# Performance work log

Hardware: AMD Instinct MI355X
Metric: run time of the kernel (lower is better)

## Reference

```python
import jax, jax.numpy as jnp
import numpy as np

N_NODES = 50000
N_EDGES = 800000
D_FEAT = 128


def setup_inputs() -> dict:
    key = jax.random.key(0)
    k1, k2, k3, k4 = jax.random.split(key, 4)
    edge_index = jax.random.randint(k1, (2, N_EDGES), 0, N_NODES, dtype=jnp.int64 if jax.config.jax_enable_x64 else jnp.int32)
    edge_vals = jax.random.uniform(k2, (N_EDGES,), dtype=jnp.float32)
    features = jax.random.normal(k3, (N_NODES, D_FEAT), dtype=jnp.float32)
    bias = jax.random.normal(k4, (D_FEAT,), dtype=jnp.float32)
    return {"edge_index": edge_index, "edge_vals": edge_vals, "features": features, "bias": bias}


def reference(edge_index, edge_vals, features, bias):
    # SpMM: out[dst] += A[dst, src] * X[src], i.e. sparse adjacency @ dense features
    src = edge_index[0]
    dst = edge_index[1]
    msg = features[src] * edge_vals[:, None]          # [E, D] gather + scale
    out = jax.ops.segment_sum(msg, dst, num_segments=features.shape[0])  # [N, D] scatter-add
    return out + bias                                  # fused bias add
```

## Files before the change

kernel.cpp:

```cpp
#include <hip/hip_runtime.h>
#include <hip/hip_bf16.h>

#define D_FEAT 128
#define D4 (D_FEAT / 4)
#define BKT_SHIFT 7
#define BKT_NODES 128
#define NCHUNK 256
#define MAXBKT 512
#define CAP 3072

__global__ __launch_bounds__(256) void k1_hist_cvt(
        const int* __restrict__ dst, int E, int chunk, int nbkt,
        int* __restrict__ M, int Mpad,
        const float4* __restrict__ fin, __hip_bfloat162* __restrict__ fout,
        int n4) {
    int c = blockIdx.x;
    int tid = threadIdx.x;
    if (c < NCHUNK) {
        __shared__ int hist[MAXBKT];
        for (int i = tid; i < nbkt; i += 256) hist[i] = 0;
        __syncthreads();
        int lo = c * chunk;
        int hi = min(lo + chunk, E);
        for (int i = lo + tid; i < hi; i += 256)
            atomicAdd(&hist[dst[i] >> BKT_SHIFT], 1);
        __syncthreads();
        for (int i = tid; i < nbkt; i += 256)
            M[i * NCHUNK + c] = hist[i];
        if (c == 0) {
            for (int i = nbkt * NCHUNK + tid; i < Mpad; i += 256) M[i] = 0;
        }
    } else {
        int nb = gridDim.x - NCHUNK;
        int idx = (c - NCHUNK) * 256 + tid;
        int stride = nb * 256;
        for (int i = idx; i < n4; i += stride) {
            float4 f = fin[i];
            fout[2 * i + 0] = __float22bfloat162_rn(make_float2(f.x, f.y));
            fout[2 * i + 1] = __float22bfloat162_rn(make_float2(f.z, f.w));
        }
    }
}

__global__ __launch_bounds__(1024) void k2a_scan(int* __restrict__ M,
                                                 int* __restrict__ bsum) {
    __shared__ int s[1024];
    int tid = threadIdx.x;
    int j = blockIdx.x * 1024 + tid;
    int v = M[j];
    s[tid] = v;
    __syncthreads();
    for (int off = 1; off < 1024; off <<= 1) {
        int t = (tid >= off) ? s[tid - off] : 0;
        __syncthreads();
        s[tid] += t;
        __syncthreads();
    }
    M[j] = s[tid] - v;
    if (tid == 1023) bsum[blockIdx.x] = s[1023];
}

__global__ void k2b_scan(int* __restrict__ bsum, int nb) {
    __shared__ int s[256];
    int tid = threadIdx.x;
    int v = (tid < nb) ? bsum[tid] : 0;
    s[tid] = v;
    __syncthreads();
    for (int off = 1; off < 256; off <<= 1) {
        int t = (tid >= off) ? s[tid - off] : 0;
        __syncthreads();
        s[tid] += t;
        __syncthreads();
    }
    if (tid < nb) bsum[tid] = s[tid] - v;
    if (tid == 255) bsum[nb] = s[255];
}

__global__ __launch_bounds__(512) void k3_partition(
        const int* __restrict__ src, const int* __restrict__ dst,
        const float* __restrict__ vals, int E, int chunk, int nbkt,
        const int* __restrict__ M, const int* __restrict__ bsum,
        int2* __restrict__ spackA) {
    __shared__ int lcur[MAXBKT];
    int c = blockIdx.x;
    int tid = threadIdx.x;
    for (int i = tid; i < nbkt; i += 512) {
        int j = i * NCHUNK + c;
        lcur[i] = M[j] + bsum[j >> 10];
    }
    __syncthreads();
    int lo = c * chunk;
    int hi = min(lo + chunk, E);
    for (int i = lo + tid; i < hi; i += 512) {
        int d = dst[i];
        int s = src[i];
        float v = vals[i];
        int pos = atomicAdd(&lcur[d >> BKT_SHIFT], 1);
        spackA[pos] = make_int2((s & 0xFFFF) | ((d & (BKT_NODES - 1)) << 16),
                                __float_as_int(v));
    }
}

__global__ __launch_bounds__(1024) void k45_sort_gather(
        const int* __restrict__ M, const int* __restrict__ bsum,
        const int2* __restrict__ spackA, int2* __restrict__ spackB,
        const __hip_bfloat162* __restrict__ feat,
        const float2* __restrict__ bias2, float2* __restrict__ out2,
        int N, int nbkt) {
    __shared__ int hist[BKT_NODES];
    __shared__ int sbuf[BKT_NODES];
    __shared__ int lcur[BKT_NODES];
    __shared__ int2 ls[CAP];
    int b = blockIdx.x;
    int tid = threadIdx.x;
    int j0 = b * NCHUNK;
    int j1 = (b + 1) * NCHUNK;
    int base = M[j0] + bsum[j0 >> 10];
    int end  = M[j1] + bsum[j1 >> 10];
    int cnt = end - base;
    bool inlds = (cnt <= CAP);

    if (tid < BKT_NODES) hist[tid] = 0;
    __syncthreads();
    for (int i = tid; i < cnt; i += 1024)
        atomicAdd(&hist[(spackA[base + i].x >> 16) & (BKT_NODES - 1)], 1);
    __syncthreads();
    if (tid < BKT_NODES) sbuf[tid] = hist[tid];
    __syncthreads();
    for (int off = 1; off < BKT_NODES; off <<= 1) {
        int t = (tid < BKT_NODES && tid >= off) ? sbuf[tid - off] : 0;
        __syncthreads();
        if (tid < BKT_NODES) sbuf[tid] += t;
        __syncthreads();
    }
    if (tid < BKT_NODES) lcur[tid] = sbuf[tid] - hist[tid];
    __syncthreads();
    for (int i = tid; i < cnt; i += 1024) {
        int2 r = spackA[base + i];
        int p = atomicAdd(&lcur[(r.x >> 16) & (BKT_NODES - 1)], 1);
        if (inlds) ls[p] = r;
        else       spackB[base + p] = r;
    }
    __syncthreads();

    int wave = tid >> 6, lane = tid & 63;
    float2 bv = bias2[lane];
    for (int n = wave; n < BKT_NODES; n += 16) {
        int node = (b << BKT_SHIFT) + n;
        if (node >= N) break;
        int lbeg = sbuf[n] - hist[n];
        int lend = sbuf[n];
        float2 acc0 = bv;
        float2 acc1 = make_float2(0.f, 0.f);
        int e = lbeg;
        if (inlds) {
            for (; e + 8 <= lend; e += 8) {
                int2 p[8];
                __hip_bfloat162 h[8];
#pragma unroll
                for (int j = 0; j < 8; j++) p[j] = ls[e + j];
#pragma unroll
                for (int j = 0; j < 8; j++)
                    h[j] = feat[(size_t)(p[j].x & 0xFFFF) * 64 + lane];
#pragma unroll
                for (int j = 0; j < 8; j++) {
                    float v = __int_as_float(p[j].y);
                    float2 f = __bfloat1622float2(h[j]);
                    if (j & 1) { acc1.x += v * f.x; acc1.y += v * f.y; }
                    else       { acc0.x += v * f.x; acc0.y += v * f.y; }
                }
            }
            for (; e < lend; e++) {
                int2 p = ls[e];
                float v = __int_as_float(p.y);
                float2 f = __bfloat1622float2(feat[(size_t)(p.x & 0xFFFF) * 64 + lane]);
                acc0.x += v * f.x; acc0.y += v * f.y;
            }
        } else {
            for (; e + 8 <= lend; e += 8) {
                int2 p[8];
                __hip_bfloat162 h[8];
#pragma unroll
                for (int j = 0; j < 8; j++) p[j] = spackB[base + e + j];
#pragma unroll
                for (int j = 0; j < 8; j++)
                    h[j] = feat[(size_t)(p[j].x & 0xFFFF) * 64 + lane];
#pragma unroll
                for (int j = 0; j < 8; j++) {
                    float v = __int_as_float(p[j].y);
                    float2 f = __bfloat1622float2(h[j]);
                    if (j & 1) { acc1.x += v * f.x; acc1.y += v * f.y; }
                    else       { acc0.x += v * f.x; acc0.y += v * f.y; }
                }
            }
            for (; e < lend; e++) {
                int2 p = spackB[base + e];
                float v = __int_as_float(p.y);
                float2 f = __bfloat1622float2(feat[(size_t)(p.x & 0xFFFF) * 64 + lane]);
                acc0.x += v * f.x; acc0.y += v * f.y;
            }
        }
        acc0.x += acc1.x; acc0.y += acc1.y;
        out2[(size_t)node * 64 + lane] = acc0;
    }
}


__global__ void init_bias_kernel(float4* __restrict__ out,
                                 const float4* __restrict__ bias, int n4) {
    int i = blockIdx.x * blockDim.x + threadIdx.x;
    if (i < n4) out[i] = bias[i & (D4 - 1)];
}

__global__ void spmm_edge_kernel(const int* __restrict__ src,
                                 const int* __restrict__ dst,
                                 const float* __restrict__ vals,
                                 const float4* __restrict__ feat,
                                 float* __restrict__ out, int n_edges) {
    int tid = blockIdx.x * blockDim.x + threadIdx.x;
    int e = tid >> 5;
    int lane = tid & 31;
    if (e >= n_edges) return;
    int s = src[e];
    int d = dst[e];
    float v = vals[e];
    float4 f = feat[(size_t)s * D4 + lane];
    float* o = out + (size_t)d * D_FEAT + lane * 4;
    atomicAdd(o + 0, v * f.x);
    atomicAdd(o + 1, v * f.y);
    atomicAdd(o + 2, v * f.z);
    atomicAdd(o + 3, v * f.w);
}

extern "C" void kernel_launch(void* const* d_in, const int* in_sizes, int n_in,
                              void* d_out, int out_size, void* d_ws, size_t ws_size,
                              hipStream_t stream) {
    const int* edge_index = (const int*)d_in[0];
    const float* edge_vals = (const float*)d_in[1];
    const float* features  = (const float*)d_in[2];
    const float* bias      = (const float*)d_in[3];

    int E = in_sizes[1];
    int N = in_sizes[2] / D_FEAT;
    const int* src = edge_index;
    const int* dst = edge_index + E;
    float* out = (float*)d_out;

    int nbkt = (N + BKT_NODES - 1) >> BKT_SHIFT;
    int n4 = N * D_FEAT / 4;
    int chunk = (E + NCHUNK - 1) / NCHUNK;
    int Mpad = ((nbkt * NCHUNK + 1 + 1023) / 1024) * 1024;
    int nblk2 = Mpad / 1024;

    size_t fb_bytes = (size_t)N * D_FEAT * 2;
    size_t sp_bytes = (size_t)E * 8;
    size_t needed = fb_bytes + 2 * sp_bytes +
                    ((size_t)Mpad + (nblk2 + 1)) * 4;

    bool ok = (ws_size >= needed) && (N >= 1) && (N <= 65536) && (E >= 1) &&
              (in_sizes[3] == D_FEAT) && (nbkt <= MAXBKT) && (nblk2 <= 256);

    if (ok) {
        char* wp = (char*)d_ws;
        __hip_bfloat162* fb16 = (__hip_bfloat162*)wp;  wp += fb_bytes;
        int2* spackA = (int2*)wp;                      wp += sp_bytes;
        int2* spackB = (int2*)wp;                      wp += sp_bytes;
        int* M       = (int*)wp;                       wp += (size_t)Mpad * 4;
        int* bsum    = (int*)wp;

        k1_hist_cvt<<<NCHUNK + 256, 256, 0, stream>>>(dst, E, chunk, nbkt,
                                                      M, Mpad,
                                                      (const float4*)features,
                                                      fb16, n4);
        k2a_scan<<<nblk2, 1024, 0, stream>>>(M, bsum);
        k2b_scan<<<1, 256, 0, stream>>>(bsum, nblk2);
        k3_partition<<<NCHUNK, 512, 0, stream>>>(src, dst, edge_vals, E, chunk,
                                                 nbkt, M, bsum, spackA);
        k45_sort_gather<<<nbkt, 1024, 0, stream>>>(M, bsum, spackA, spackB,
                                                   fb16, (const float2*)bias,
                                                   (float2*)out, N, nbkt);
    } else {
        int no4 = out_size / 4;
        {
            int block = 256, grid = (no4 + block - 1) / block;
            init_bias_kernel<<<grid, block, 0, stream>>>((float4*)out,
                                                         (const float4*)bias, no4);
        }
        {
            int block = 256;
            long long total = (long long)E * 32;
            int grid = (int)((total + block - 1) / block);
            spmm_edge_kernel<<<grid, block, 0, stream>>>(src, dst, edge_vals,
                                                         (const float4*)features,
                                                         out, E);
        }
    }
}
```

Baseline: 145.6 us.

## Fold bucket prefix scan into partition kernel, dropping two scan launches

Removes the two separate scan kernels. Each partition block now reads the full chunk-by-bucket histogram (stored chunk-major, MAXBKT wide), computes bucket totals and its own chunk prefix, and does a block-level scan to get bucket offsets. Block 0 publishes global bucket bases for the sort/gather kernel. This cuts two kernel launches and their serialization, in exchange for every partition block redundantly reading 256x512 histogram entries and scanning them.

```diff
diff --git a/kernel.cpp b/kernel.cpp
--- a/kernel.cpp
+++ b/kernel.cpp
@@ -10,26 +10,24 @@
 #define CAP 3072
 
 __global__ __launch_bounds__(256) void k1_hist_cvt(
-        const int* __restrict__ dst, int E, int chunk, int nbkt,
-        int* __restrict__ M, int Mpad,
+        const int* __restrict__ dst, int E, int nbkt,
+        int* __restrict__ M,
         const float4* __restrict__ fin, __hip_bfloat162* __restrict__ fout,
         int n4) {
     int c = blockIdx.x;
     int tid = threadIdx.x;
     if (c < NCHUNK) {
         __shared__ int hist[MAXBKT];
-        for (int i = tid; i < nbkt; i += 256) hist[i] = 0;
-        __syncthreads();
+        for (int i = tid; i < MAXBKT; i += 256) hist[i] = 0;
+        __syncthreads();
+        int chunk = (E + NCHUNK - 1) / NCHUNK;
         int lo = c * chunk;
         int hi = min(lo + chunk, E);
         for (int i = lo + tid; i < hi; i += 256)
             atomicAdd(&hist[dst[i] >> BKT_SHIFT], 1);
         __syncthreads();
-        for (int i = tid; i < nbkt; i += 256)
-            M[i * NCHUNK + c] = hist[i];
-        if (c == 0) {
-            for (int i = nbkt * NCHUNK + tid; i < Mpad; i += 256) M[i] = 0;
-        }
+        for (int i = tid; i < MAXBKT; i += 256)
+            M[c * MAXBKT + i] = hist[i];
     } else {
         int nb = gridDim.x - NCHUNK;
         int idx = (c - NCHUNK) * 256 + tid;
@@ -42,67 +40,50 @@
     }
 }
 
-__global__ __launch_bounds__(1024) void k2a_scan(int* __restrict__ M,
-                                                 int* __restrict__ bsum) {
-    __shared__ int s[1024];
-    int tid = threadIdx.x;
-    int j = blockIdx.x * 1024 + tid;
-    int v = M[j];
-    s[tid] = v;
-    __syncthreads();
-    for (int off = 1; off < 1024; off <<= 1) {
-        int t = (tid >= off) ? s[tid - off] : 0;
-        __syncthreads();
-        s[tid] += t;
-        __syncthreads();
-    }
-    M[j] = s[tid] - v;
-    if (tid == 1023) bsum[blockIdx.x] = s[1023];
-}
-
-__global__ void k2b_scan(int* __restrict__ bsum, int nb) {
-    __shared__ int s[256];
-    int tid = threadIdx.x;
-    int v = (tid < nb) ? bsum[tid] : 0;
-    s[tid] = v;
-    __syncthreads();
-    for (int off = 1; off < 256; off <<= 1) {
-        int t = (tid >= off) ? s[tid - off] : 0;
-        __syncthreads();
-        s[tid] += t;
-        __syncthreads();
-    }
-    if (tid < nb) bsum[tid] = s[tid] - v;
-    if (tid == 255) bsum[nb] = s[255];
-}
-
 __global__ __launch_bounds__(512) void k3_partition(
         const int* __restrict__ src, const int* __restrict__ dst,
-        const float* __restrict__ vals, int E, int chunk, int nbkt,
-        const int* __restrict__ M, const int* __restrict__ bsum,
+        const float* __restrict__ vals, int E, int nbkt,
+        const int* __restrict__ M, int* __restrict__ gbase,
         int2* __restrict__ spackA) {
+    __shared__ int s[MAXBKT];
     __shared__ int lcur[MAXBKT];
     int c = blockIdx.x;
     int tid = threadIdx.x;
-    for (int i = tid; i < nbkt; i += 512) {
-        int j = i * NCHUNK + c;
-        lcur[i] = M[j] + bsum[j >> 10];
-    }
-    __syncthreads();
+    int tot = 0, pre = 0;
+    for (int cc = 0; cc < NCHUNK; ++cc) {
+        int m = M[cc * MAXBKT + tid];
+        tot += m;
+        pre += (cc < c) ? m : 0;
+    }
+    s[tid] = tot;
+    __syncthreads();
+    for (int off = 1; off < MAXBKT; off <<= 1) {
+        int t = (tid >= off) ? s[tid - off] : 0;
+        __syncthreads();
+        s[tid] += t;
+        __syncthreads();
+    }
+    int incl = s[tid];
+    int base = incl - tot;
+    lcur[tid] = base + pre;
+    if (c == 0) {
+        if (tid < nbkt) gbase[tid] = base;
+        if (tid == MAXBKT - 1) gbase[nbkt] = incl;
+    }
+    __syncthreads();
+    int chunk = (E + NCHUNK - 1) / NCHUNK;
     int lo = c * chunk;
     int hi = min(lo + chunk, E);
     for (int i = lo + tid; i < hi; i += 512) {
         int d = dst[i];
-        int s = src[i];
-        float v = vals[i];
         int pos = atomicAdd(&lcur[d >> BKT_SHIFT], 1);
-        spackA[pos] = make_int2((s & 0xFFFF) | ((d & (BKT_NODES - 1)) << 16),
-                                __float_as_int(v));
+        spackA[pos] = make_int2((src[i] & 0xFFFF) | ((d & (BKT_NODES - 1)) << 16),
+                                __float_as_int(vals[i]));
     }
 }
 
 __global__ __launch_bounds__(1024) void k45_sort_gather(
-        const int* __restrict__ M, const int* __restrict__ bsum,
+        const int* __restrict__ gbase,
         const int2* __restrict__ spackA, int2* __restrict__ spackB,
         const __hip_bfloat162* __restrict__ feat,
         const float2* __restrict__ bias2, float2* __restrict__ out2,
@@ -113,10 +94,8 @@
     __shared__ int2 ls[CAP];
     int b = blockIdx.x;
     int tid = threadIdx.x;
-    int j0 = b * NCHUNK;
-    int j1 = (b + 1) * NCHUNK;
-    int base = M[j0] + bsum[j0 >> 10];
-    int end  = M[j1] + bsum[j1 >> 10];
+    int base = gbase[b];
+    int end  = gbase[b + 1];
     int cnt = end - base;
     bool inlds = (cnt <= CAP);
 
@@ -248,35 +227,29 @@
 
     int nbkt = (N + BKT_NODES - 1) >> BKT_SHIFT;
     int n4 = N * D_FEAT / 4;
-    int chunk = (E + NCHUNK - 1) / NCHUNK;
-    int Mpad = ((nbkt * NCHUNK + 1 + 1023) / 1024) * 1024;
-    int nblk2 = Mpad / 1024;
 
     size_t fb_bytes = (size_t)N * D_FEAT * 2;
     size_t sp_bytes = (size_t)E * 8;
-    size_t needed = fb_bytes + 2 * sp_bytes +
-                    ((size_t)Mpad + (nblk2 + 1)) * 4;
+    size_t m_bytes  = (size_t)NCHUNK * MAXBKT * 4;
+    size_t needed = fb_bytes + 2 * sp_bytes + m_bytes + (MAXBKT + 1) * 4;
 
     bool ok = (ws_size >= needed) && (N >= 1) && (N <= 65536) && (E >= 1) &&
-              (in_sizes[3] == D_FEAT) && (nbkt <= MAXBKT) && (nblk2 <= 256);
+              (in_sizes[3] == D_FEAT) && (nbkt <= MAXBKT);
 
     if (ok) {
         char* wp = (char*)d_ws;
         __hip_bfloat162* fb16 = (__hip_bfloat162*)wp;  wp += fb_bytes;
         int2* spackA = (int2*)wp;                      wp += sp_bytes;
         int2* spackB = (int2*)wp;                      wp += sp_bytes;
-        int* M       = (int*)wp;                       wp += (size_t)Mpad * 4;
-        int* bsum    = (int*)wp;
-
-        k1_hist_cvt<<<NCHUNK + 256, 256, 0, stream>>>(dst, E, chunk, nbkt,
-                                                      M, Mpad,
+        int* M       = (int*)wp;                       wp += m_bytes;
+        int* gbase   = (int*)wp;
+
+        k1_hist_cvt<<<NCHUNK + 256, 256, 0, stream>>>(dst, E, nbkt, M,
                                                       (const float4*)features,
                                                       fb16, n4);
-        k2a_scan<<<nblk2, 1024, 0, stream>>>(M, bsum);
-        k2b_scan<<<1, 256, 0, stream>>>(bsum, nblk2);
-        k3_partition<<<NCHUNK, 512, 0, stream>>>(src, dst, edge_vals, E, chunk,
-                                                 nbkt, M, bsum, spackA);
-        k45_sort_gather<<<nbkt, 1024, 0, stream>>>(M, bsum, spackA, spackB,
+        k3_partition<<<NCHUNK, 512, 0, stream>>>(src, dst, edge_vals, E,
+                                                 nbkt, M, gbase, spackA);
+        k45_sort_gather<<<nbkt, 1024, 0, stream>>>(gbase, spackA, spackB,
                                                    fb16, (const float2*)bias,
                                                    (float2*)out, N, nbkt);
     } else {
```

New measurement: 152.5 us. +4.7%, slower.
